# Optimization experiments

Hardware: AMD Instinct MI355X
Metric: run time of the kernel (lower is better)

The kernel has to match this reference:

```python
import jax, jax.numpy as jnp
import numpy as np

ENC_IN = 512
D_MODEL = 1024
EMB_DIM = 32
IN_DIM = D_MODEL + EMB_DIM  # 1056
BATCH = 64


def setup_inputs() -> dict:
    key = jax.random.key(0)
    ks = jax.random.split(key, 12)
    s = 0.02
    return {
        "x": jax.random.normal(ks[0], (BATCH, ENC_IN, D_MODEL), dtype=jnp.float32),
        "emb": jax.random.normal(ks[1], (ENC_IN, EMB_DIM), dtype=jnp.float32) * s,
        # weights stored [in, out] (transposed vs torch Linear, same math)
        "w1": jax.random.normal(ks[2], (IN_DIM, IN_DIM), dtype=jnp.float32) * s,
        "b1": jnp.zeros((IN_DIM,), dtype=jnp.float32),
        "wq": jax.random.normal(ks[3], (IN_DIM, IN_DIM), dtype=jnp.float32) * s,
        "bq": jnp.zeros((IN_DIM,), dtype=jnp.float32),
        "wk": jax.random.normal(ks[4], (IN_DIM, IN_DIM), dtype=jnp.float32) * s,
        "bk": jnp.zeros((IN_DIM,), dtype=jnp.float32),
        "wv": jax.random.normal(ks[5], (IN_DIM, IN_DIM), dtype=jnp.float32) * s,
        "bv": jnp.zeros((IN_DIM,), dtype=jnp.float32),
        "w2": jax.random.normal(ks[6], (IN_DIM, D_MODEL), dtype=jnp.float32) * s,
        "b2": jnp.zeros((D_MODEL,), dtype=jnp.float32),
    }


def reference(x, emb, w1, b1, wq, bq, wk, bk, wv, bv, w2, b2):
    B = x.shape[0]
    # variable embedding: same for every batch element -> broadcast concat
    e = jnp.broadcast_to(emb[None, :, :], (B, ENC_IN, EMB_DIM))
    h = jnp.concatenate([x, e], axis=2)                      # [B, S, IN_DIM]
    h = jax.nn.leaky_relu(h @ w1 + b1, negative_slope=0.2)   # l1
    # hand-rolled self-attention: no scaling, softmax over last dim
    q = h @ wq + bq
    k = h @ wk + bk
    v = h @ wv + bv
    energy = jnp.einsum("bsd,btd->bst", q, k)                # [B, S, S]
    attn = jax.nn.softmax(energy, axis=-1)
    out = jnp.einsum("bst,btd->bsd", attn, v)                # [B, S, IN_DIM]
    return out @ w2 + b2                                     # [B, S, D_MODEL]
```

## Files before the change

### kernel.cpp

```cpp
#include <hip/hip_runtime.h>
#include <hip/hip_bf16.h>
#include <cstdint>

typedef __hip_bfloat16 bf16;
typedef __attribute__((ext_vector_type(8))) short short8;
typedef __attribute__((ext_vector_type(4))) float f32x4;

__device__ __forceinline__ void gload16(const bf16* g, bf16* l) {
    __builtin_amdgcn_global_load_lds(
        (__attribute__((address_space(1))) void*)g,
        (__attribute__((address_space(3))) void*)l, 16, 0, 0);
}
#define VMC(n) asm volatile("s_waitcnt vmcnt(" #n ")" ::: "memory")
__device__ __forceinline__ void bar() {
    asm volatile("" ::: "memory");
    __builtin_amdgcn_s_barrier();
    asm volatile("" ::: "memory");
}

__device__ __forceinline__ void stage_half(const bf16* __restrict__ G, int ld,
                                           int row0, int k0, bf16* lregion,
                                           int w, int lrow, int lslot)
{
    const bf16* s0 = G + (long long)(row0 + w * 8 + lrow) * ld + (k0 + lslot * 8);
    gload16(s0, lregion + (w * 64) * 8);
    gload16(s0 + (long long)64 * ld, lregion + (512 + w * 64) * 8);
}

#define LOAD_AI(dst, i_, mh, P) do { \
    _Pragma("unroll") for (int ks_ = 0; ks_ < 2; ++ks_) \
      dst[i_][ks_] = *(const short8*)((P) + ((mh) * 64 + (i_) * 16 + l15) * 64 \
                                         + (((ks_ * 4 + lq) ^ l7) * 8)); } while (0)
#define LOAD_B(nh, dst) do { _Pragma("unroll") for (int j_ = 0; j_ < 2; ++j_) { \
    _Pragma("unroll") for (int ks_ = 0; ks_ < 2; ++ks_) \
      dst[j_][ks_] = *(const short8*)(pb + (bhr + (nh) * 32 + j_ * 16 + l15) * 64 \
                                         + (((ks_ * 4 + lq) ^ l7) * 8)); } } while (0)
#define DO_Q(mh, nh, AF, BF) do { \
    __builtin_amdgcn_s_setprio(1); \
    _Pragma("unroll") for (int i_ = 0; i_ < 4; ++i_) \
      _Pragma("unroll") for (int j_ = 0; j_ < 2; ++j_) \
        _Pragma("unroll") for (int ks_ = 0; ks_ < 2; ++ks_) \
          acc[mh][nh][i_][j_] = __builtin_amdgcn_mfma_f32_16x16x32_bf16( \
              AF[i_][ks_], BF[j_][ks_], acc[mh][nh][i_][j_], 0, 0, 0); \
    __builtin_amdgcn_s_setprio(0); \
} while (0)

template<int OUT_BF16, int ACT, int BIASMODE, int ROUTE>
__global__ __launch_bounds__(512, 2)
void gemm256(const bf16* __restrict__ Abase, const bf16* __restrict__ Bbase,
             void* __restrict__ Cbase, const float* __restrict__ bias,
             int K, int lda, int ldb, int ldc, int nwrite,
             long long sA, long long sB, long long sC, long long segStride)
{
    __shared__ bf16 lds[2][2][2][8192];

    const int gx = gridDim.x, gy = gridDim.y;
    const int nwg = gx * gy * gridDim.z;
    const int lin = blockIdx.x + gx * (blockIdx.y + gy * blockIdx.z);
    const int qch = nwg >> 3, rch = nwg & 7;
    const int xcd = lin & 7, pos = lin >> 3;
    const int nl = (xcd < rch ? xcd * (qch + 1)
                              : rch * (qch + 1) + (xcd - rch) * qch) + pos;
    const int bz = nl / (gx * gy);
    const int rem = nl - bz * (gx * gy);
    const int by = rem / gx;
    const int bx = rem - by * gx;

    const int tid = threadIdx.x;
    const int wid = tid >> 6, lane = tid & 63;
    const int wm = wid >> 2, wn = wid & 3;
    const int l15 = lane & 15, l7 = lane & 7, lq = lane >> 4;
    const int lrow = lane >> 3, lslot = l7 ^ lrow;
    const int bhr = (wn & 1) * 64;

    const bf16* A = Abase + (long long)bz * sA;
    const bf16* B = Bbase + (long long)bz * sB;
    const int brow = by * 256, bcol = bx * 256;

    f32x4 acc[2][2][4][2] = {};
    short8 aFe[4][2], aFo[4][2], bF0[2][2], bF1[2][2];

    const int nt = K >> 6;

    stage_half(B, ldb, bcol,       0,  &lds[0][1][0][0], wid, lrow, lslot);
    stage_half(B, ldb, bcol + 128, 0,  &lds[0][1][1][0], wid, lrow, lslot);
    stage_half(A, lda, brow,       0,  &lds[0][0][0][0], wid, lrow, lslot);
    stage_half(A, lda, brow + 128, 0,  &lds[0][0][1][0], wid, lrow, lslot);
    stage_half(B, ldb, bcol,       64, &lds[1][1][0][0], wid, lrow, lslot);
    stage_half(B, ldb, bcol + 128, 64, &lds[1][1][1][0], wid, lrow, lslot);
    VMC(4);
    bar();

    for (int t = 0; t < nt; ++t) {
        const int b = t & 1;
        const bf16* pa = &lds[b][0][wm][0];
        const bf16* pb = &lds[b][1][wn >> 1][0];
        bf16* oA = &lds[b ^ 1][0][0][0];
        bf16* cB = &lds[b][1][0][0];
        const int t1 = (t + 1 == nt) ? 0 : t + 1;
        const int t2 = (t + 2 >= nt) ? t + 2 - nt : t + 2;
        const int k1 = t1 << 6, k2 = t2 << 6;

        LOAD_B(0, bF0);
        LOAD_AI(aFe, 0, 0, pa); LOAD_AI(aFe, 1, 0, pa);
        LOAD_AI(aFe, 2, 0, pa); LOAD_AI(aFe, 3, 0, pa);
        LOAD_B(1, bF1);
        stage_half(A, lda, brow, k1, oA, wid, lrow, lslot);
        bar();
        DO_Q(0, 0, aFe, bF0);
        bar();

        LOAD_AI(aFo, 0, 1, pa); LOAD_AI(aFo, 1, 1, pa);
        stage_half(A, lda, brow + 128, k1, oA + 8192, wid, lrow, lslot);
        bar();
        DO_Q(0, 1, aFe, bF1);
        bar();

        LOAD_AI(aFo, 2, 1, pa); LOAD_AI(aFo, 3, 1, pa);
        stage_half(B, ldb, bcol, k2, cB, wid, lrow, lslot);
        bar();
        DO_Q(1, 1, aFo, bF1);
        bar();

        stage_half(B, ldb, bcol + 128, k2, cB + 8192, wid, lrow, lslot);
        bar();
        DO_Q(1, 0, aFo, bF0);
        VMC(4);
        bar();
    }
    VMC(0);

    const long long cofs0 = (long long)bz * sC;
    #pragma unroll
    for (int mh = 0; mh < 2; ++mh)
      #pragma unroll
      for (int nh = 0; nh < 2; ++nh)
        #pragma unroll
        for (int i = 0; i < 4; ++i)
          #pragma unroll
          for (int j = 0; j < 2; ++j) {
              const int gc = bcol + wn * 64 + nh * 32 + j * 16 + l15;
              const bool wr = gc < nwrite;
              const int row0 = brow + wm * 128 + mh * 64 + i * 16 + lq * 4;
              if (wr) {
                  float bvv = 0.0f;
                  if (BIASMODE == 1) bvv = bias[gc];
                  if (BIASMODE == 3) bvv = bias[(long long)bz * 512 + gc];
                  long long base; int lc, ld;
                  if (ROUTE == 2) {
                      if (gc < 1152) { base = 0; lc = gc; ld = 1152; }
                      else { base = segStride; lc = gc - 1152; ld = 1088; }
                  } else { base = cofs0; lc = gc; ld = ldc; }
                  #pragma unroll
                  for (int rr = 0; rr < 4; ++rr) {
                      float vv = acc[mh][nh][i][j][rr] + bvv;
                      if (ACT) vv = vv > 0.0f ? vv : 0.2f * vv;
                      const long long cidx = base + (long long)(row0 + rr) * ld + lc;
                      if (OUT_BF16) ((bf16*)Cbase)[cidx] = (bf16)vv;
                      else          ((float*)Cbase)[cidx] = vv;
                  }
              }
          }
}

__global__ void concat_cast_kernel(const float* __restrict__ x,
                                   const float* __restrict__ emb,
                                   bf16* __restrict__ out)
{
    const int m = blockIdx.x;
    const int s = m & 511;
    const float* xr = x + (long long)m * 1024;
    bf16* orow = out + (long long)m * 1088;
    for (int g = threadIdx.x; g < 272; g += 256) {
        const int c = g * 4;
        float4 v;
        if (c < 1024)      v = *(const float4*)&xr[c];
        else if (c < 1056) v = *(const float4*)&emb[s * 32 + (c - 1024)];
        else               v = make_float4(0.f, 0.f, 0.f, 0.f);
        bf16 t[4] = { (bf16)v.x, (bf16)v.y, (bf16)v.z, (bf16)v.w };
        *(ushort4*)&orow[c] = *(ushort4*)t;
    }
}

__global__ void wtrans3_kernel(const float* __restrict__ w1, const float* __restrict__ wv,
                               const float* __restrict__ w2,
                               bf16* __restrict__ w1T, bf16* __restrict__ Bqv,
                               bf16* __restrict__ w2T)
{
    const int z = blockIdx.z;
    const float* src; bf16* dst; int NIN, NP, srcld;
    switch (z) {
        case 0: src = w1; dst = w1T; NIN = 1056; NP = 1280; srcld = 1056; break;
        case 1: src = wv; dst = Bqv; NIN = 1056; NP = 1152; srcld = 1056; break;
        default: src = w2; dst = w2T; NIN = 1024; NP = 1024; srcld = 1024; break;
    }
    const int KIN = 1056, KP = 1088;
    const int k0 = blockIdx.x * 32, n0 = blockIdx.y * 32;
    if (n0 >= NP) return;
    __shared__ float t[32][33];
    const int tx = threadIdx.x, ty = threadIdx.y;
    const int kk = k0 + ty, nn = n0 + tx;
    t[ty][tx] = (kk < KIN && nn < NIN) ? src[(long long)kk * srcld + nn] : 0.0f;
    __syncthreads();
    const int ko = k0 + tx, no = n0 + ty;
    if (no < NP && ko < KP)
        dst[(long long)no * KP + ko] = (bf16)t[tx][ty];
}

__global__ void wcast2_kernel(const float* __restrict__ wq, const float* __restrict__ wk,
                              bf16* __restrict__ wqC, bf16* __restrict__ wkC)
{
    const int i = blockIdx.x;
    const float* src = blockIdx.y ? wk : wq;
    bf16* dst = blockIdx.y ? wkC : wqC;
    for (int c = threadIdx.x; c < 1088; c += 256) {
        float v = (i < 1056 && c < 1056) ? src[(long long)i * 1056 + c] : 0.0f;
        dst[(long long)i * 1088 + c] = (bf16)v;
    }
}

__global__ void uvec_kernel(const float* __restrict__ wk, const float* __restrict__ bq,
                            float* __restrict__ u)
{
    const int wid = threadIdx.x >> 6, lane = threadIdx.x & 63;
    const int e = blockIdx.x * 4 + wid;
    if (e >= 1088) return;
    float s = 0.0f;
    if (e < 1056) {
        for (int d = lane; d < 1056; d += 64)
            s += wk[(long long)e * 1056 + d] * bq[d];
    }
    #pragma unroll
    for (int sh = 32; sh > 0; sh >>= 1) s += __shfl_xor(s, sh);
    if (lane == 0) u[e] = s;
}

__global__ __launch_bounds__(256)
void cvec_kernel(const bf16* __restrict__ h, const float* __restrict__ u,
                 float* __restrict__ c)
{
    const int wid = threadIdx.x >> 6, lane = threadIdx.x & 63;
    const long long row = (long long)blockIdx.x * 4 + wid;
    const bf16* hr = h + row * 1088;
    float s = 0.0f;
    #pragma unroll
    for (int j = 0; j < 17; ++j)
        s += (float)hr[j * 64 + lane] * u[j * 64 + lane];
    #pragma unroll
    for (int sh = 32; sh > 0; sh >>= 1) s += __shfl_xor(s, sh);
    if (lane == 0) c[row] = s;
}

__global__ void biasprep_kernel(const float* __restrict__ b1, const float* __restrict__ bv,
                                const float* __restrict__ b2,
                                float* __restrict__ b1p, float* __restrict__ bqv2,
                                float* __restrict__ b2p)
{
    const int i = blockIdx.x * 256 + threadIdx.x;
    if (i < 1088) {
        b1p[i] = (i < 1056) ? b1[i] : 0.0f;
    } else if (i < 1088 + 2304) {
        const int j = i - 1088;
        bqv2[j] = (j < 1056) ? bv[j] : 0.0f;
    } else if (i < 1088 + 2304 + 1024) {
        b2p[i - (1088 + 2304)] = b2[i - (1088 + 2304)];
    }
}

__global__ void vtrans_kernel(const bf16* __restrict__ v, bf16* __restrict__ vt)
{
    __shared__ bf16 t[64][72];
    const long long b = blockIdx.z;
    const bf16* vb = v + b * (512LL * 1152);
    bf16* vtb = vt + b * (1280LL * 512);
    const int d0 = blockIdx.x * 64, s0 = blockIdx.y * 64;
    const int tx = threadIdx.x & 15, ty = threadIdx.x >> 4;
    const bool zz = d0 >= 1152;
    #pragma unroll
    for (int i = 0; i < 4; ++i) {
        const int row = ty + i * 16;
        ushort4 val = make_ushort4(0, 0, 0, 0);
        if (!zz)
            val = *(const ushort4*)&vb[(long long)(s0 + row) * 1152 + d0 + tx * 4];
        *(ushort4*)&t[row][tx * 4] = val;
    }
    __syncthreads();
    #pragma unroll
    for (int i = 0; i < 4; ++i) {
        const int d = ty + i * 16;
        ushort4 o;
        o.x = *(const ushort*)&t[tx * 4 + 0][d];
        o.y = *(const ushort*)&t[tx * 4 + 1][d];
        o.z = *(const ushort*)&t[tx * 4 + 2][d];
        o.w = *(const ushort*)&t[tx * 4 + 3][d];
        *(ushort4*)&vtb[(long long)(d0 + d) * 512 + s0 + tx * 4] = o;
    }
}

__global__ __launch_bounds__(256)
void softmax_kernel(const float* __restrict__ e, bf16* __restrict__ p)
{
    const int wid = threadIdx.x >> 6, lane = threadIdx.x & 63;
    const long long row = (long long)blockIdx.x * 4 + wid;
    const float* er = e + row * 512;
    float v[8];
    float mx = -3.0e38f;
    #pragma unroll
    for (int j = 0; j < 8; ++j) { v[j] = er[j * 64 + lane]; mx = fmaxf(mx, v[j]); }
    #pragma unroll
    for (int s = 32; s > 0; s >>= 1) mx = fmaxf(mx, __shfl_xor(mx, s));
    float sum = 0.0f;
    #pragma unroll
    for (int j = 0; j < 8; ++j) { v[j] = __expf(v[j] - mx); sum += v[j]; }
    #pragma unroll
    for (int s = 32; s > 0; s >>= 1) sum += __shfl_xor(sum, s);
    const float inv = 1.0f / sum;
    bf16* pr = p + row * 512;
    #pragma unroll
    for (int j = 0; j < 8; ++j) pr[j * 64 + lane] = (bf16)(v[j] * inv);
}

extern "C" void kernel_launch(void* const* d_in, const int* in_sizes, int n_in,
                              void* d_out, int out_size, void* d_ws, size_t ws_size,
                              hipStream_t stream)
{
    const float* x   = (const float*)d_in[0];
    const float* emb = (const float*)d_in[1];
    const float* w1  = (const float*)d_in[2];
    const float* b1  = (const float*)d_in[3];
    const float* wq  = (const float*)d_in[4];
    const float* bq  = (const float*)d_in[5];
    const float* wk  = (const float*)d_in[6];
    const float* wv  = (const float*)d_in[8];
    const float* bv  = (const float*)d_in[9];
    const float* w2  = (const float*)d_in[10];
    const float* b2  = (const float*)d_in[11];
    float* out = (float*)d_out;

    const long long Mrows = 32768;
    const int KR = 1088;

    char* ws = (char*)d_ws;
    size_t off = 0;
    auto alloc = [&](size_t bytes) -> char* {
        char* p = ws + off;
        off += (bytes + 255) & ~(size_t)255;
        return p;
    };
    char* R1   = alloc((size_t)Mrows * KR * 2);
    char* Rh   = alloc((size_t)Mrows * KR * 2);
    char* Rq   = alloc((size_t)Mrows * KR * 2);
    bf16* vbuf = (bf16*)alloc((size_t)Mrows * 1152 * 2);
    bf16* vT   = (bf16*)alloc((size_t)64 * 1280 * 512 * 2);
    bf16* w1T  = (bf16*)alloc((size_t)1280 * KR * 2);
    bf16* Bqv  = (bf16*)alloc((size_t)2432 * KR * 2);
    bf16* w2T  = (bf16*)alloc((size_t)1024 * KR * 2);
    bf16* wqC  = (bf16*)alloc((size_t)1280 * KR * 2);
    bf16* wkC  = (bf16*)alloc((size_t)1280 * KR * 2);
    float* b1p  = (float*)alloc((size_t)1088 * 4);
    float* bqv2 = (float*)alloc((size_t)2304 * 4);
    float* b2p  = (float*)alloc((size_t)1024 * 4);
    float* uvec = (float*)alloc((size_t)1088 * 4);
    float* cvec = (float*)alloc((size_t)Mrows * 4);

    bf16*  hcat   = (bf16*)R1;
    float* energy = (float*)R1;
    bf16*  pv     = (bf16*)R1;
    bf16*  h      = (bf16*)Rh;
    bf16*  qbuf   = (bf16*)Rq;
    bf16*  attn   = (bf16*)Rq;

    concat_cast_kernel<<<32768, 256, 0, stream>>>(x, emb, hcat);
    wtrans3_kernel<<<dim3(34, 40, 3), dim3(32, 32), 0, stream>>>(
        w1, wv, w2, w1T, Bqv, w2T);
    wcast2_kernel<<<dim3(1280, 2), 256, 0, stream>>>(wq, wk, wqC, wkC);
    uvec_kernel<<<272, 256, 0, stream>>>(wk, bq, uvec);
    biasprep_kernel<<<18, 256, 0, stream>>>(b1, bv, b2, b1p, bqv2, b2p);

    gemm256<1, 0, 0, 0><<<dim3(5, 5, 1), 512, 0, stream>>>(
        wkC, wqC, Bqv + 1152LL * KR, nullptr, KR, KR, KR, KR, KR, 0, 0, 0, 0);
    gemm256<1, 1, 1, 0><<<dim3(5, 128, 1), 512, 0, stream>>>(
        hcat, w1T, h, b1p, KR, KR, KR, KR, KR, 0, 0, 0, 0);
    cvec_kernel<<<8192, 256, 0, stream>>>(h, uvec, cvec);
    gemm256<1, 0, 1, 2><<<dim3(9, 128, 1), 512, 0, stream>>>(
        h, Bqv, vbuf, bqv2, KR, KR, KR, 0, 2240, 0, 0, 0,
        (long long)(qbuf - vbuf));
    vtrans_kernel<<<dim3(20, 8, 64), 256, 0, stream>>>(vbuf, vT);
    gemm256<0, 0, 3, 0><<<dim3(2, 2, 64), 512, 0, stream>>>(
        qbuf, h, energy, cvec, KR, KR, KR, 512, 512,
        512LL * KR, 512LL * KR, 512LL * 512, 0);
    softmax_kernel<<<8192, 256, 0, stream>>>(energy, attn);
    gemm256<1, 0, 0, 0><<<dim3(5, 2, 64), 512, 0, stream>>>(
        attn, vT, pv, nullptr, 512, 512, 512, KR, KR,
        512LL * 512, 1280LL * 512, 512LL * KR, 0);
    gemm256<0, 0, 1, 0><<<dim3(4, 128, 1), 512, 0, stream>>>(
        pv, w2T, out, b2p, KR, KR, KR, 1024, 1024, 0, 0, 0, 0);
}
```

Measured before the change: 633.5 us.

## Fuse fp32 concat-cast of x/emb into first GEMM A-tile staging

Removes the standalone concat_cast kernel: the l1 GEMM now loads fp32 x and emb directly, casts to bf16 in registers and writes the A tile to LDS with explicit lgkmcnt waits. It also merges the wq/wk cast kernel into the weight transpose kernel, saving one launch. The aim is to avoid writing and re-reading the 64x512x1088 bf16 intermediate. In exchange, the A-tile loads become synchronous register loads instead of async global-to-LDS loads, and they are re-read by each of the 5 column blocks, which may stall the MFMA pipeline.

```diff
diff --git a/kernel.cpp b/kernel.cpp
--- a/kernel.cpp
+++ b/kernel.cpp
@@ -12,6 +12,7 @@
         (__attribute__((address_space(3))) void*)l, 16, 0, 0);
 }
 #define VMC(n) asm volatile("s_waitcnt vmcnt(" #n ")" ::: "memory")
+#define LGKM0 asm volatile("s_waitcnt lgkmcnt(0)" ::: "memory")
 __device__ __forceinline__ void bar() {
     asm volatile("" ::: "memory");
     __builtin_amdgcn_s_barrier();
@@ -25,6 +26,39 @@
     const bf16* s0 = G + (long long)(row0 + w * 8 + lrow) * ld + (k0 + lslot * 8);
     gload16(s0, lregion + (w * 64) * 8);
     gload16(s0 + (long long)64 * ld, lregion + (512 + w * 64) * 8);
+}
+
+__device__ __forceinline__ void stage_cast_row(
+    const float* __restrict__ X, const float* __restrict__ E,
+    int row, int c, bf16* dst)
+{
+    float v[8] = {0.f, 0.f, 0.f, 0.f, 0.f, 0.f, 0.f, 0.f};
+    if (c < 1024) {
+        const float4 a = *(const float4*)&X[(long long)row * 1024 + c];
+        const float4 b = *(const float4*)&X[(long long)row * 1024 + c + 4];
+        v[0] = a.x; v[1] = a.y; v[2] = a.z; v[3] = a.w;
+        v[4] = b.x; v[5] = b.y; v[6] = b.z; v[7] = b.w;
+    } else if (c < 1056) {
+        const int s = row & 511;
+        const float4 a = *(const float4*)&E[s * 32 + (c - 1024)];
+        const float4 b = *(const float4*)&E[s * 32 + (c - 1024) + 4];
+        v[0] = a.x; v[1] = a.y; v[2] = a.z; v[3] = a.w;
+        v[4] = b.x; v[5] = b.y; v[6] = b.z; v[7] = b.w;
+    }
+    bf16 t[8];
+    #pragma unroll
+    for (int z = 0; z < 8; ++z) t[z] = (bf16)v[z];
+    *(short8*)dst = *(short8*)t;
+}
+
+__device__ __forceinline__ void stage_cast_half(
+    const float* __restrict__ X, const float* __restrict__ E,
+    int row0, int k0, bf16* lregion, int w, int lrow, int lslot, int lane)
+{
+    const int c = k0 + lslot * 8;
+    const int r = row0 + w * 8 + lrow;
+    stage_cast_row(X, E, r,      c, lregion + w * 512 + lane * 8);
+    stage_cast_row(X, E, r + 64, c, lregion + 4096 + w * 512 + lane * 8);
 }
 
 #define LOAD_AI(dst, i_, mh, P) do { \
@@ -45,10 +79,11 @@
     __builtin_amdgcn_s_setprio(0); \
 } while (0)
 
-template<int OUT_BF16, int ACT, int BIASMODE, int ROUTE>
+template<int OUT_BF16, int ACT, int BIASMODE, int ROUTE, int CASTA>
 __global__ __launch_bounds__(512, 2)
 void gemm256(const bf16* __restrict__ Abase, const bf16* __restrict__ Bbase,
              void* __restrict__ Cbase, const float* __restrict__ bias,
+             const float* __restrict__ Xsrc, const float* __restrict__ Esrc,
              int K, int lda, int ldb, int ldc, int nwrite,
              long long sA, long long sB, long long sC, long long segStride)
 {
@@ -84,11 +119,17 @@
 
     stage_half(B, ldb, bcol,       0,  &lds[0][1][0][0], wid, lrow, lslot);
     stage_half(B, ldb, bcol + 128, 0,  &lds[0][1][1][0], wid, lrow, lslot);
-    stage_half(A, lda, brow,       0,  &lds[0][0][0][0], wid, lrow, lslot);
-    stage_half(A, lda, brow + 128, 0,  &lds[0][0][1][0], wid, lrow, lslot);
+    if (CASTA) {
+        stage_cast_half(Xsrc, Esrc, brow,       0, &lds[0][0][0][0], wid, lrow, lslot, lane);
+        stage_cast_half(Xsrc, Esrc, brow + 128, 0, &lds[0][0][1][0], wid, lrow, lslot, lane);
+    } else {
+        stage_half(A, lda, brow,       0,  &lds[0][0][0][0], wid, lrow, lslot);
+        stage_half(A, lda, brow + 128, 0,  &lds[0][0][1][0], wid, lrow, lslot);
+    }
     stage_half(B, ldb, bcol,       64, &lds[1][1][0][0], wid, lrow, lslot);
     stage_half(B, ldb, bcol + 128, 64, &lds[1][1][1][0], wid, lrow, lslot);
     VMC(4);
+    if (CASTA) LGKM0;
     bar();
 
     for (int t = 0; t < nt; ++t) {
@@ -105,15 +146,19 @@
         LOAD_AI(aFe, 0, 0, pa); LOAD_AI(aFe, 1, 0, pa);
         LOAD_AI(aFe, 2, 0, pa); LOAD_AI(aFe, 3, 0, pa);
         LOAD_B(1, bF1);
-        stage_half(A, lda, brow, k1, oA, wid, lrow, lslot);
+        if (CASTA) stage_cast_half(Xsrc, Esrc, brow, k1, oA, wid, lrow, lslot, lane);
+        else       stage_half(A, lda, brow, k1, oA, wid, lrow, lslot);
         bar();
         DO_Q(0, 0, aFe, bF0);
+        if (CASTA) LGKM0;
         bar();
 
         LOAD_AI(aFo, 0, 1, pa); LOAD_AI(aFo, 1, 1, pa);
-        stage_half(A, lda, brow + 128, k1, oA + 8192, wid, lrow, lslot);
+        if (CASTA) stage_cast_half(Xsrc, Esrc, brow + 128, k1, oA + 8192, wid, lrow, lslot, lane);
+        else       stage_half(A, lda, brow + 128, k1, oA + 8192, wid, lrow, lslot);
         bar();
         DO_Q(0, 1, aFe, bF1);
+        if (CASTA) LGKM0;
         bar();
 
         LOAD_AI(aFo, 2, 1, pa); LOAD_AI(aFo, 3, 1, pa);
@@ -163,31 +208,25 @@
           }
 }
 
-__global__ void concat_cast_kernel(const float* __restrict__ x,
-                                   const float* __restrict__ emb,
-                                   bf16* __restrict__ out)
-{
-    const int m = blockIdx.x;
-    const int s = m & 511;
-    const float* xr = x + (long long)m * 1024;
-    bf16* orow = out + (long long)m * 1088;
-    for (int g = threadIdx.x; g < 272; g += 256) {
-        const int c = g * 4;
-        float4 v;
-        if (c < 1024)      v = *(const float4*)&xr[c];
-        else if (c < 1056) v = *(const float4*)&emb[s * 32 + (c - 1024)];
-        else               v = make_float4(0.f, 0.f, 0.f, 0.f);
-        bf16 t[4] = { (bf16)v.x, (bf16)v.y, (bf16)v.z, (bf16)v.w };
-        *(ushort4*)&orow[c] = *(ushort4*)t;
-    }
-}
-
-__global__ void wtrans3_kernel(const float* __restrict__ w1, const float* __restrict__ wv,
-                               const float* __restrict__ w2,
-                               bf16* __restrict__ w1T, bf16* __restrict__ Bqv,
-                               bf16* __restrict__ w2T)
+__global__ void wprep_kernel(const float* __restrict__ w1, const float* __restrict__ wv,
+                             const float* __restrict__ w2, const float* __restrict__ wq,
+                             const float* __restrict__ wk,
+                             bf16* __restrict__ w1T, bf16* __restrict__ Bqv,
+                             bf16* __restrict__ w2T, bf16* __restrict__ wqC,
+                             bf16* __restrict__ wkC)
 {
     const int z = blockIdx.z;
+    const int tx = threadIdx.x, ty = threadIdx.y;
+    if (z >= 3) {
+        const float* src = (z == 3) ? wq : wk;
+        bf16* dst = (z == 3) ? wqC : wkC;
+        const int r = blockIdx.y * 32 + ty, c = blockIdx.x * 32 + tx;
+        if (r < 1280 && c < 1088) {
+            float v = (r < 1056 && c < 1056) ? src[(long long)r * 1056 + c] : 0.0f;
+            dst[(long long)r * 1088 + c] = (bf16)v;
+        }
+        return;
+    }
     const float* src; bf16* dst; int NIN, NP, srcld;
     switch (z) {
         case 0: src = w1; dst = w1T; NIN = 1056; NP = 1280; srcld = 1056; break;
@@ -198,25 +237,12 @@
     const int k0 = blockIdx.x * 32, n0 = blockIdx.y * 32;
     if (n0 >= NP) return;
     __shared__ float t[32][33];
-    const int tx = threadIdx.x, ty = threadIdx.y;
     const int kk = k0 + ty, nn = n0 + tx;
     t[ty][tx] = (kk < KIN && nn < NIN) ? src[(long long)kk * srcld + nn] : 0.0f;
     __syncthreads();
     const int ko = k0 + tx, no = n0 + ty;
     if (no < NP && ko < KP)
         dst[(long long)no * KP + ko] = (bf16)t[tx][ty];
-}
-
-__global__ void wcast2_kernel(const float* __restrict__ wq, const float* __restrict__ wk,
-                              bf16* __restrict__ wqC, bf16* __restrict__ wkC)
-{
-    const int i = blockIdx.x;
-    const float* src = blockIdx.y ? wk : wq;
-    bf16* dst = blockIdx.y ? wkC : wqC;
-    for (int c = threadIdx.x; c < 1088; c += 256) {
-        float v = (i < 1056 && c < 1056) ? src[(long long)i * 1056 + c] : 0.0f;
-        dst[(long long)i * 1088 + c] = (bf16)v;
-    }
 }
 
 __global__ void uvec_kernel(const float* __restrict__ wk, const float* __restrict__ bq,
@@ -363,36 +389,36 @@
     float* uvec = (float*)alloc((size_t)1088 * 4);
     float* cvec = (float*)alloc((size_t)Mrows * 4);
 
-    bf16*  hcat   = (bf16*)R1;
     float* energy = (float*)R1;
     bf16*  pv     = (bf16*)R1;
     bf16*  h      = (bf16*)Rh;
     bf16*  qbuf   = (bf16*)Rq;
     bf16*  attn   = (bf16*)Rq;
 
-    concat_cast_kernel<<<32768, 256, 0, stream>>>(x, emb, hcat);
-    wtrans3_kernel<<<dim3(34, 40, 3), dim3(32, 32), 0, stream>>>(
-        w1, wv, w2, w1T, Bqv, w2T);
-    wcast2_kernel<<<dim3(1280, 2), 256, 0, stream>>>(wq, wk, wqC, wkC);
+    wprep_kernel<<<dim3(34, 40, 5), dim3(32, 32), 0, stream>>>(
+        w1, wv, w2, wq, wk, w1T, Bqv, w2T, wqC, wkC);
     uvec_kernel<<<272, 256, 0, stream>>>(wk, bq, uvec);
     biasprep_kernel<<<18, 256, 0, stream>>>(b1, bv, b2, b1p, bqv2, b2p);
 
-    gemm256<1, 0, 0, 0><<<dim3(5, 5, 1), 512, 0, stream>>>(
-        wkC, wqC, Bqv + 1152LL * KR, nullptr, KR, KR, KR, KR, KR, 0, 0, 0, 0);
-    gemm256<1, 1, 1, 0><<<dim3(5, 128, 1), 512, 0, stream>>>(
-        hcat, w1T, h, b1p, KR, KR, KR, KR, KR, 0, 0, 0, 0);
+    gemm256<1, 0, 0, 0, 0><<<dim3(5, 5, 1), 512, 0, stream>>>(
+        wkC, wqC, Bqv + 1152LL * KR, nullptr, nullptr, nullptr,
+        KR, KR, KR, KR, KR, 0, 0, 0, 0);
+    gemm256<1, 1, 1, 0, 1><<<dim3(5, 128, 1), 512, 0, stream>>>(
+        nullptr, w1T, h, b1p, x, emb,
+        KR, 1024, KR, KR, KR, 0, 0, 0, 0);
     cvec_kernel<<<8192, 256, 0, stream>>>(h, uvec, cvec);
-    gemm256<1, 0, 1, 2><<<dim3(9, 128, 1), 512, 0, stream>>>(
-        h, Bqv, vbuf, bqv2, KR, KR, KR, 0, 2240, 0, 0, 0,
-        (long long)(qbuf - vbuf));
+    gemm256<1, 0, 1, 2, 0><<<dim3(9, 128, 1), 512, 0, stream>>>(
+        h, Bqv, vbuf, bqv2, nullptr, nullptr,
+        KR, KR, KR, 0, 2240, 0, 0, 0, (long long)(qbuf - vbuf));
     vtrans_kernel<<<dim3(20, 8, 64), 256, 0, stream>>>(vbuf, vT);
-    gemm256<0, 0, 3, 0><<<dim3(2, 2, 64), 512, 0, stream>>>(
-        qbuf, h, energy, cvec, KR, KR, KR, 512, 512,
-        512LL * KR, 512LL * KR, 512LL * 512, 0);
+    gemm256<0, 0, 3, 0, 0><<<dim3(2, 2, 64), 512, 0, stream>>>(
+        qbuf, h, energy, cvec, nullptr, nullptr,
+        KR, KR, KR, 512, 512, 512LL * KR, 512LL * KR, 512LL * 512, 0);
     softmax_kernel<<<8192, 256, 0, stream>>>(energy, attn);
-    gemm256<1, 0, 0, 0><<<dim3(5, 2, 64), 512, 0, stream>>>(
-        attn, vT, pv, nullptr, 512, 512, 512, KR, KR,
-        512LL * 512, 1280LL * 512, 512LL * KR, 0);
-    gemm256<0, 0, 1, 0><<<dim3(4, 128, 1), 512, 0, stream>>>(
-        pv, w2T, out, b2p, KR, KR, KR, 1024, 1024, 0, 0, 0, 0);
-}
+    gemm256<1, 0, 0, 0, 0><<<dim3(5, 2, 64), 512, 0, stream>>>(
+        attn, vT, pv, nullptr, nullptr, nullptr,
+        512, 512, 512, KR, KR, 512LL * 512, 1280LL * 512, 512LL * KR, 0);
+    gemm256<0, 0, 1, 0, 0><<<dim3(4, 128, 1), 512, 0, stream>>>(
+        pv, w2T, out, b2p, nullptr, nullptr,
+        KR, KR, KR, 1024, 1024, 0, 0, 0, 0);
+}
```

Result: slower. 721.5 us (+13.9%).

## Write V transposed directly from QV GEMM epilogue and merge weight prep kernels

Applied to the files above, without the earlier changes.

The fused h·[Wv|WqWk^T] GEMM epilogue now stores the V columns straight into the transposed per-batch vT layout with 4-wide packed stores, which removes the separate vbuf buffer and the vtrans kernel. A small kernel zeroes the padded rows of vT. The wq/wk cast kernel is folded into the weight transpose launch as extra z-slices. This saves a full read and write of V, but the transposed epilogue stores are strided across rows of vT and may coalesce poorly.

```diff
diff --git a/kernel.cpp b/kernel.cpp
--- a/kernel.cpp
+++ b/kernel.cpp
@@ -146,18 +146,28 @@
                   float bvv = 0.0f;
                   if (BIASMODE == 1) bvv = bias[gc];
                   if (BIASMODE == 3) bvv = bias[(long long)bz * 512 + gc];
-                  long long base; int lc, ld;
-                  if (ROUTE == 2) {
-                      if (gc < 1152) { base = 0; lc = gc; ld = 1152; }
-                      else { base = segStride; lc = gc - 1152; ld = 1088; }
-                  } else { base = cofs0; lc = gc; ld = ldc; }
-                  #pragma unroll
-                  for (int rr = 0; rr < 4; ++rr) {
-                      float vv = acc[mh][nh][i][j][rr] + bvv;
-                      if (ACT) vv = vv > 0.0f ? vv : 0.2f * vv;
-                      const long long cidx = base + (long long)(row0 + rr) * ld + lc;
-                      if (OUT_BF16) ((bf16*)Cbase)[cidx] = (bf16)vv;
-                      else          ((float*)Cbase)[cidx] = vv;
+                  if (ROUTE == 2 && gc < 1152) {
+                      const int b_ = row0 >> 9, s_ = row0 & 511;
+                      bf16 t4[4];
+                      #pragma unroll
+                      for (int rr = 0; rr < 4; ++rr) {
+                          float vv = acc[mh][nh][i][j][rr] + bvv;
+                          t4[rr] = (bf16)vv;
+                      }
+                      *(ushort4*)&((bf16*)Cbase)[((long long)b_ * 1280 + gc) * 512 + s_]
+                          = *(ushort4*)t4;
+                  } else {
+                      long long base; int lc, ld;
+                      if (ROUTE == 2) { base = segStride; lc = gc - 1152; ld = 1088; }
+                      else { base = cofs0; lc = gc; ld = ldc; }
+                      #pragma unroll
+                      for (int rr = 0; rr < 4; ++rr) {
+                          float vv = acc[mh][nh][i][j][rr] + bvv;
+                          if (ACT) vv = vv > 0.0f ? vv : 0.2f * vv;
+                          const long long cidx = base + (long long)(row0 + rr) * ld + lc;
+                          if (OUT_BF16) ((bf16*)Cbase)[cidx] = (bf16)vv;
+                          else          ((float*)Cbase)[cidx] = vv;
+                      }
                   }
               }
           }
@@ -182,12 +192,25 @@
     }
 }
 
-__global__ void wtrans3_kernel(const float* __restrict__ w1, const float* __restrict__ wv,
-                               const float* __restrict__ w2,
-                               bf16* __restrict__ w1T, bf16* __restrict__ Bqv,
-                               bf16* __restrict__ w2T)
+__global__ void wprep_kernel(const float* __restrict__ w1, const float* __restrict__ wv,
+                             const float* __restrict__ w2, const float* __restrict__ wq,
+                             const float* __restrict__ wk,
+                             bf16* __restrict__ w1T, bf16* __restrict__ Bqv,
+                             bf16* __restrict__ w2T, bf16* __restrict__ wqC,
+                             bf16* __restrict__ wkC)
 {
     const int z = blockIdx.z;
+    const int tx = threadIdx.x, ty = threadIdx.y;
+    if (z >= 3) {
+        const float* src = (z == 3) ? wq : wk;
+        bf16* dst = (z == 3) ? wqC : wkC;
+        const int r = blockIdx.y * 32 + ty, c = blockIdx.x * 32 + tx;
+        if (r < 1280 && c < 1088) {
+            float v = (r < 1056 && c < 1056) ? src[(long long)r * 1056 + c] : 0.0f;
+            dst[(long long)r * 1088 + c] = (bf16)v;
+        }
+        return;
+    }
     const float* src; bf16* dst; int NIN, NP, srcld;
     switch (z) {
         case 0: src = w1; dst = w1T; NIN = 1056; NP = 1280; srcld = 1056; break;
@@ -198,7 +221,6 @@
     const int k0 = blockIdx.x * 32, n0 = blockIdx.y * 32;
     if (n0 >= NP) return;
     __shared__ float t[32][33];
-    const int tx = threadIdx.x, ty = threadIdx.y;
     const int kk = k0 + ty, nn = n0 + tx;
     t[ty][tx] = (kk < KIN && nn < NIN) ? src[(long long)kk * srcld + nn] : 0.0f;
     __syncthreads();
@@ -207,16 +229,16 @@
         dst[(long long)no * KP + ko] = (bf16)t[tx][ty];
 }
 
-__global__ void wcast2_kernel(const float* __restrict__ wq, const float* __restrict__ wk,
-                              bf16* __restrict__ wqC, bf16* __restrict__ wkC)
-{
-    const int i = blockIdx.x;
-    const float* src = blockIdx.y ? wk : wq;
-    bf16* dst = blockIdx.y ? wkC : wqC;
-    for (int c = threadIdx.x; c < 1088; c += 256) {
-        float v = (i < 1056 && c < 1056) ? src[(long long)i * 1056 + c] : 0.0f;
-        dst[(long long)i * 1088 + c] = (bf16)v;
-    }
+__global__ void vtzero_kernel(bf16* __restrict__ vt)
+{
+    const long long i = ((long long)blockIdx.x * 256 + threadIdx.x) * 8;
+    const int per_batch = 128 * 512;
+    const int b = (int)(i / per_batch);
+    const long long r = i - (long long)b * per_batch;
+    ushort4 z4 = make_ushort4(0, 0, 0, 0);
+    bf16* p = &vt[(long long)b * (1280LL * 512) + 1152LL * 512 + r];
+    *(ushort4*)p = z4;
+    *(ushort4*)(p + 4) = z4;
 }
 
 __global__ void uvec_kernel(const float* __restrict__ wk, const float* __restrict__ bq,
@@ -264,36 +286,6 @@
         bqv2[j] = (j < 1056) ? bv[j] : 0.0f;
     } else if (i < 1088 + 2304 + 1024) {
         b2p[i - (1088 + 2304)] = b2[i - (1088 + 2304)];
-    }
-}
-
-__global__ void vtrans_kernel(const bf16* __restrict__ v, bf16* __restrict__ vt)
-{
-    __shared__ bf16 t[64][72];
-    const long long b = blockIdx.z;
-    const bf16* vb = v + b * (512LL * 1152);
-    bf16* vtb = vt + b * (1280LL * 512);
-    const int d0 = blockIdx.x * 64, s0 = blockIdx.y * 64;
-    const int tx = threadIdx.x & 15, ty = threadIdx.x >> 4;
-    const bool zz = d0 >= 1152;
-    #pragma unroll
-    for (int i = 0; i < 4; ++i) {
-        const int row = ty + i * 16;
-        ushort4 val = make_ushort4(0, 0, 0, 0);
-        if (!zz)
-            val = *(const ushort4*)&vb[(long long)(s0 + row) * 1152 + d0 + tx * 4];
-        *(ushort4*)&t[row][tx * 4] = val;
-    }
-    __syncthreads();
-    #pragma unroll
-    for (int i = 0; i < 4; ++i) {
-        const int d = ty + i * 16;
-        ushort4 o;
-        o.x = *(const ushort*)&t[tx * 4 + 0][d];
-        o.y = *(const ushort*)&t[tx * 4 + 1][d];
-        o.z = *(const ushort*)&t[tx * 4 + 2][d];
-        o.w = *(const ushort*)&t[tx * 4 + 3][d];
-        *(ushort4*)&vtb[(long long)(d0 + d) * 512 + s0 + tx * 4] = o;
     }
 }
 
@@ -350,7 +342,6 @@
     char* R1   = alloc((size_t)Mrows * KR * 2);
     char* Rh   = alloc((size_t)Mrows * KR * 2);
     char* Rq   = alloc((size_t)Mrows * KR * 2);
-    bf16* vbuf = (bf16*)alloc((size_t)Mrows * 1152 * 2);
     bf16* vT   = (bf16*)alloc((size_t)64 * 1280 * 512 * 2);
     bf16* w1T  = (bf16*)alloc((size_t)1280 * KR * 2);
     bf16* Bqv  = (bf16*)alloc((size_t)2432 * KR * 2);
@@ -371,21 +362,21 @@
     bf16*  attn   = (bf16*)Rq;
 
     concat_cast_kernel<<<32768, 256, 0, stream>>>(x, emb, hcat);
-    wtrans3_kernel<<<dim3(34, 40, 3), dim3(32, 32), 0, stream>>>(
-        w1, wv, w2, w1T, Bqv, w2T);
-    wcast2_kernel<<<dim3(1280, 2), 256, 0, stream>>>(wq, wk, wqC, wkC);
+    wprep_kernel<<<dim3(34, 40, 5), dim3(32, 32), 0, stream>>>(
+        w1, wv, w2, wq, wk, w1T, Bqv, w2T, wqC, wkC);
     uvec_kernel<<<272, 256, 0, stream>>>(wk, bq, uvec);
     biasprep_kernel<<<18, 256, 0, stream>>>(b1, bv, b2, b1p, bqv2, b2p);
+    vtzero_kernel<<<2048, 256, 0, stream>>>(vT);
 
     gemm256<1, 0, 0, 0><<<dim3(5, 5, 1), 512, 0, stream>>>(
-        wkC, wqC, Bqv + 1152LL * KR, nullptr, KR, KR, KR, KR, KR, 0, 0, 0, 0);
+        wkC, wqC, Bqv + 1152LL * KR, nullptr,
+        KR, KR, KR, KR, KR, 0, 0, 0, 0);
     gemm256<1, 1, 1, 0><<<dim3(5, 128, 1), 512, 0, stream>>>(
         hcat, w1T, h, b1p, KR, KR, KR, KR, KR, 0, 0, 0, 0);
     cvec_kernel<<<8192, 256, 0, stream>>>(h, uvec, cvec);
     gemm256<1, 0, 1, 2><<<dim3(9, 128, 1), 512, 0, stream>>>(
-        h, Bqv, vbuf, bqv2, KR, KR, KR, 0, 2240, 0, 0, 0,
-        (long long)(qbuf - vbuf));
-    vtrans_kernel<<<dim3(20, 8, 64), 256, 0, stream>>>(vbuf, vT);
+        h, Bqv, vT, bqv2, KR, KR, KR, 0, 2240, 0, 0, 0,
+        (long long)(qbuf - vT));
     gemm256<0, 0, 3, 0><<<dim3(2, 2, 64), 512, 0, stream>>>(
         qbuf, h, energy, cvec, KR, KR, KR, 512, 512,
         512LL * KR, 512LL * KR, 512LL * 512, 0);
```

Result: faster. 600.7 us (-5.2%).
